# Kernel optimization log

Hardware: AMD Instinct MI355X
Metric: run time of the kernel (lower is better)

Reference implementation:

```python
import jax, jax.numpy as jnp
import numpy as np

D_MODEL = 2048
N_HEADS = 16
D_K = D_MODEL // N_HEADS
MAX_SEQ_LEN = 2048


def _rotary_tables(dim, max_seq_len):
    angular_freq = (1.0 / 10000.0) ** jnp.linspace(0.0, 1.0, dim // 2, dtype=jnp.float32)
    t = jnp.arange(max_seq_len, dtype=jnp.float32)
    theta = jnp.einsum('i,j->ij', t, angular_freq)  # [S, dk/2]
    return jnp.cos(theta), jnp.sin(theta)


def _apply_rotary(x, cos, sin):
    # x: [B, H, S, dk]; cos/sin: [S, dk/2]
    seq_len = x.shape[-2]
    c = cos[:seq_len][None, None]
    s = sin[:seq_len][None, None]
    x1, x2 = jnp.split(x, 2, axis=-1)
    y1 = x1 * c - x2 * s
    y2 = x1 * s + x2 * c
    return jnp.concatenate([y1, y2], axis=-1).astype(x.dtype)


def setup_inputs() -> dict:
    key = jax.random.key(0)
    k_x, k_qkv, k_o = jax.random.split(key, 3)
    B, S = 2, 2048
    x = jax.random.normal(k_x, (B, S, D_MODEL), dtype=jnp.float32)
    scale = 1.0 / np.sqrt(D_MODEL)
    w_qkv = jax.random.normal(k_qkv, (3 * D_MODEL, D_MODEL), dtype=jnp.float32) * scale
    w_o = jax.random.normal(k_o, (D_MODEL, D_MODEL), dtype=jnp.float32) * scale
    return {"x": x, "w_qkv": w_qkv, "w_o": w_o}


def reference(x, w_qkv, w_o):
    B, S, _ = x.shape
    cos, sin = _rotary_tables(D_K, MAX_SEQ_LEN)
    qkv = jnp.einsum('bsd,ed->bse', x, w_qkv)  # [B, S, 3*d_model]
    qkv = qkv.reshape(B, S, 3, N_HEADS, D_K).transpose(2, 0, 3, 1, 4)  # [3,B,H,S,dk]
    Q, K, V = qkv[0], qkv[1], qkv[2]
    Q = _apply_rotary(Q, cos, sin)
    K = _apply_rotary(K, cos, sin)
    scale = 1.0 / np.sqrt(D_K)
    scores = jnp.einsum('bhqd,bhkd->bhqk', Q, K) * scale
    causal = jnp.tril(jnp.ones((S, S), dtype=bool))
    scores = jnp.where(causal[None, None], scores, jnp.finfo(scores.dtype).min)
    attn = jax.nn.softmax(scores, axis=-1)
    out = jnp.einsum('bhqk,bhkd->bhqd', attn, V)  # [B,H,S,dk]
    out = out.transpose(0, 2, 1, 3).reshape(B, S, D_MODEL)
    return jnp.einsum('bsd,ed->bse', out, w_o)
```

## Files before the change

kernel.cpp:

```cpp
#include <hip/hip_runtime.h>
#include <hip/hip_bf16.h>


typedef __bf16 bf16;
typedef __bf16 bf16x4 __attribute__((ext_vector_type(4)));
typedef __bf16 bf16x8 __attribute__((ext_vector_type(8)));
typedef float f32x4 __attribute__((ext_vector_type(4)));
typedef float f32x16 __attribute__((ext_vector_type(16)));
typedef int i32x4 __attribute__((ext_vector_type(4)));

#define DEV __device__ __forceinline__

DEV void gll16(const void* g, void* lds_base_wave_uniform) {
  __builtin_amdgcn_global_load_lds((const __attribute__((address_space(1))) void*)g,
                                   (__attribute__((address_space(3))) void*)lds_base_wave_uniform,
                                   16, 0, 0);
}

DEV f32x4 mfma16(bf16x8 a, bf16x8 b, f32x4 c) {
  return __builtin_amdgcn_mfma_f32_16x16x32_bf16(a, b, c, 0, 0, 0);
}
DEV f32x16 mfma32(bf16x8 a, bf16x8 b, f32x16 c) {
  return __builtin_amdgcn_mfma_f32_32x32x16_bf16(a, b, c, 0, 0, 0);
}

DEV int pack2(float x, float y) {
  union { bf16 h[2]; int i; } u;
  u.h[0] = (bf16)x; u.h[1] = (bf16)y;
  return u.i;
}

__global__ __launch_bounds__(256) void cvt_f32_bf16(const float* __restrict__ in,
                                                    bf16* __restrict__ out, int n) {
  int i = (blockIdx.x * 256 + threadIdx.x) << 3;
  if (i >= n) return;
  float4 a = *(const float4*)(in + i);
  float4 b = *(const float4*)(in + i + 4);
  bf16x8 o;
  o[0] = (bf16)a.x; o[1] = (bf16)a.y; o[2] = (bf16)a.z; o[3] = (bf16)a.w;
  o[4] = (bf16)b.x; o[5] = (bf16)b.y; o[6] = (bf16)b.z; o[7] = (bf16)b.w;
  *(bf16x8*)(out + i) = o;
}

__global__ __launch_bounds__(256) void rope_table(float* __restrict__ ctab,
                                                  float* __restrict__ stab) {
  int id = blockIdx.x * 256 + threadIdx.x;
  int s = id >> 6, j = id & 63;
  float freq = powf(10000.0f, -(float)j / 63.0f);
  float th = (float)s * freq;
  ctab[id] = cosf(th);
  stab[id] = sinf(th);
}

__global__ __launch_bounds__(256) void rope_apply(bf16* __restrict__ Qb, bf16* __restrict__ Kb,
                                                  const float* __restrict__ ctab,
                                                  const float* __restrict__ stab) {
  const float QSCALE = 0.08838834764831845f * 1.4426950408889634f;
  int id = blockIdx.x * 256 + threadIdx.x;
  const int half = 32 * 2048 * 8;
  bf16* P = (id < half) ? Qb : Kb;
  const float scale = (id < half) ? QSCALE : 1.0f;
  int t = (id < half) ? id : id - half;
  const int d0 = (t & 7) << 3;
  const int s = (t >> 3) & 2047;
  const int bh = t >> 14;
  bf16* p = P + (((size_t)bh * 2048 + s) << 7);
  bf16x8 x1 = *(bf16x8*)(p + d0);
  bf16x8 x2 = *(bf16x8*)(p + d0 + 64);
  float4 ca = *(const float4*)(ctab + (s << 6) + d0);
  float4 cb = *(const float4*)(ctab + (s << 6) + d0 + 4);
  float4 sa = *(const float4*)(stab + (s << 6) + d0);
  float4 sb = *(const float4*)(stab + (s << 6) + d0 + 4);
  const float c[8] = {ca.x, ca.y, ca.z, ca.w, cb.x, cb.y, cb.z, cb.w};
  const float sn[8] = {sa.x, sa.y, sa.z, sa.w, sb.x, sb.y, sb.z, sb.w};
  bf16x8 y1, y2;
#pragma unroll
  for (int j = 0; j < 8; ++j) {
    const float a = (float)x1[j], b = (float)x2[j];
    y1[j] = (bf16)((a * c[j] - b * sn[j]) * scale);
    y2[j] = (bf16)((a * sn[j] + b * c[j]) * scale);
  }
  *(bf16x8*)(p + d0) = y1;
  *(bf16x8*)(p + d0 + 64) = y2;
}

__global__ __launch_bounds__(512, 2) void gemm384(const bf16* __restrict__ A,
                                                  const bf16* __restrict__ Bt,
                                                  bf16* __restrict__ q_out,
                                                  bf16* __restrict__ k_out,
                                                  bf16* __restrict__ v_out) {
  constexpr int K = 2048, NKT = 64;
  constexpr int BUFB = 40960;
  __shared__ char lds[3 * BUFB];
  const int id = blockIdx.x;
  const int swz = (id & 7) * 32 + (id >> 3);
  const int bx = swz & 15, by = swz >> 4;
  const int m0 = by << 8;
  const int n0 = bx * 384;
  const int tid = threadIdx.x, w = tid >> 6, l = tid & 63;
  const int wm = w >> 2, wn = w & 3;
  const int lsl = (l & 7) ^ ((l >> 3) & 7);
  const int srow = ((l >> 3) << 1) + (lsl >> 2);
  const int scol = (lsl & 3) << 3;

  auto STAGE = [&](int t, char* base) {
    const int k0 = t << 5;
#pragma unroll
    for (int c = 0; c < 2; ++c) {
      const int row = (c << 7) + (w << 4) + srow;
      gll16(A + (size_t)(m0 + row) * K + k0 + scol, base + (c << 13) + (w << 10));
    }
#pragma unroll
    for (int c = 0; c < 3; ++c) {
      const int row = (c << 7) + (w << 4) + srow;
      gll16(Bt + (size_t)(n0 + row) * K + k0 + scol, base + 16384 + (c << 13) + (w << 10));
    }
  };

  f32x4 acc[8][6] = {};

  STAGE(0, (char*)lds);
  STAGE(1, (char*)lds + BUFB);
  asm volatile("s_waitcnt vmcnt(5)" ::: "memory");
  __builtin_amdgcn_s_barrier();

#pragma unroll 1
  for (int t = 0, bi = 0, bj = 2; t < NKT; ++t) {
    char* rbase = (char*)lds + bi * BUFB;
    bf16x8 bfr[6];
#pragma unroll
    for (int j = 0; j < 6; ++j) {
      const int row = wn * 96 + (j << 4) + (l & 15);
      const int sr = row >> 1;
      bfr[j] = *(const bf16x8*)(rbase + 16384 + sr * 128 +
                                (((((row & 1) << 2) | (l >> 4)) ^ (sr & 7)) << 4));
    }
    bf16x8 af[4];
#pragma unroll
    for (int i = 0; i < 4; ++i) {
      const int row = (wm << 7) + (i << 4) + (l & 15);
      const int sr = row >> 1;
      af[i] = *(const bf16x8*)(rbase + sr * 128 +
                               (((((row & 1) << 2) | (l >> 4)) ^ (sr & 7)) << 4));
    }
    if (t + 2 < NKT) STAGE(t + 2, (char*)lds + bj * BUFB);
    asm volatile("s_waitcnt lgkmcnt(0)" ::: "memory");
    __builtin_amdgcn_sched_barrier(0);
    __builtin_amdgcn_s_setprio(1);
#pragma unroll
    for (int i = 0; i < 4; ++i)
#pragma unroll
      for (int j = 0; j < 6; ++j)
        acc[i][j] = mfma16(af[i], bfr[j], acc[i][j]);
    __builtin_amdgcn_s_setprio(0);
#pragma unroll
    for (int i = 0; i < 4; ++i) {
      const int row = (wm << 7) + 64 + (i << 4) + (l & 15);
      const int sr = row >> 1;
      af[i] = *(const bf16x8*)(rbase + sr * 128 +
                               (((((row & 1) << 2) | (l >> 4)) ^ (sr & 7)) << 4));
    }
    asm volatile("s_waitcnt lgkmcnt(0)" ::: "memory");
    __builtin_amdgcn_sched_barrier(0);
    __builtin_amdgcn_s_setprio(1);
#pragma unroll
    for (int i = 0; i < 4; ++i)
#pragma unroll
      for (int j = 0; j < 6; ++j)
        acc[4 + i][j] = mfma16(af[i], bfr[j], acc[4 + i][j]);
    __builtin_amdgcn_s_setprio(0);
    if (t + 2 < NKT) {
      asm volatile("s_waitcnt vmcnt(5)" ::: "memory");
    } else if (t + 2 == NKT) {
      asm volatile("s_waitcnt vmcnt(0)" ::: "memory");
    }
    __builtin_amdgcn_sched_barrier(0);
    __builtin_amdgcn_s_barrier();
    bi = (bi == 2) ? 0 : bi + 1;
    bj = (bj == 2) ? 0 : bj + 1;
  }

#pragma unroll
  for (int i = 0; i < 8; ++i)
#pragma unroll
    for (int j = 0; j < 6; ++j) {
      const int nl = n0 + wn * 96 + (j << 4) + (l & 15);
      const int which = nl >> 11;
      const int h = (nl >> 7) & 15, d = nl & 127;
      if (which < 2) {
        bf16* dst = which ? k_out : q_out;
#pragma unroll
        for (int r = 0; r < 4; ++r) {
          const int m = m0 + (wm << 7) + (i << 4) + ((l >> 4) << 2) + r;
          const int b_ = m >> 11, s = m & 2047;
          dst[(((size_t)((b_ << 4) | h)) * 2048 + s) * 128 + d] = (bf16)acc[i][j][r];
        }
      } else {
        const int sb = m0 + (wm << 7) + (i << 4) + ((l >> 4) << 2);
        const int b_ = sb >> 11, s = sb & 2047;
        bf16x4 vv;
#pragma unroll
        for (int r = 0; r < 4; ++r) vv[r] = (bf16)acc[i][j][r];
        *(bf16x4*)(v_out + ((size_t)((b_ << 4) | h) << 18) + ((size_t)d << 11) + s) = vv;
      }
    }
}

template <int NTN>
__global__ __launch_bounds__(256, 2) void gemm_o(const bf16* __restrict__ A,
                                                 const bf16* __restrict__ Bt,
                                                 float* __restrict__ f_out) {
  constexpr int K = 2048, NKT = 64;
  constexpr int BUFB = 16384;
  __shared__ char lds[3 * BUFB];
  const int nwg = 32 * NTN;
  const int id = blockIdx.x;
  const int swz = (id & 7) * (nwg >> 3) + (id >> 3);
  const int bx = swz % NTN, by = swz / NTN;
  const int m0 = by << 7, n0 = bx << 7;
  const int tid = threadIdx.x, w = tid >> 6, l = tid & 63;
  const int wm = w >> 1, wn = w & 1;
  const int lsl = (l & 7) ^ ((l >> 3) & 7);
  const int srow = ((l >> 3) << 1) + (lsl >> 2);
  const int scol = (lsl & 3) << 3;

  auto STAGE = [&](int t, char* base) {
    const int k0 = t << 5;
#pragma unroll
    for (int c = 0; c < 2; ++c) {
      const int row = (c << 6) + (w << 4) + srow;
      gll16(A + (size_t)(m0 + row) * K + k0 + scol, base + (c << 12) + (w << 10));
      gll16(Bt + (size_t)(n0 + row) * K + k0 + scol, base + 8192 + (c << 12) + (w << 10));
    }
  };

  f32x4 acc[4][4] = {};

  STAGE(0, (char*)lds);
  STAGE(1, (char*)lds + BUFB);
  asm volatile("s_waitcnt vmcnt(4)" ::: "memory");
  __builtin_amdgcn_s_barrier();

#pragma unroll 1
  for (int t = 0, bi = 0, bj = 2; t < NKT; ++t) {
    char* rbase = (char*)lds + bi * BUFB;
    bf16x8 af[4], bfr[4];
#pragma unroll
    for (int i = 0; i < 4; ++i) {
      const int row = (wm << 6) + (i << 4) + (l & 15);
      const int sr = row >> 1;
      af[i] = *(const bf16x8*)(rbase + sr * 128 +
                               (((((row & 1) << 2) | (l >> 4)) ^ (sr & 7)) << 4));
    }
#pragma unroll
    for (int j = 0; j < 4; ++j) {
      const int row = (wn << 6) + (j << 4) + (l & 15);
      const int sr = row >> 1;
      bfr[j] = *(const bf16x8*)(rbase + 8192 + sr * 128 +
                                (((((row & 1) << 2) | (l >> 4)) ^ (sr & 7)) << 4));
    }
    if (t + 2 < NKT) STAGE(t + 2, (char*)lds + bj * BUFB);
    asm volatile("s_waitcnt lgkmcnt(0)" ::: "memory");
    __builtin_amdgcn_sched_barrier(0);
    __builtin_amdgcn_s_setprio(1);
#pragma unroll
    for (int i = 0; i < 4; ++i)
#pragma unroll
      for (int j = 0; j < 4; ++j)
        acc[i][j] = mfma16(af[i], bfr[j], acc[i][j]);
    __builtin_amdgcn_s_setprio(0);
    if (t + 2 < NKT) {
      asm volatile("s_waitcnt vmcnt(4)" ::: "memory");
    } else if (t + 2 == NKT) {
      asm volatile("s_waitcnt vmcnt(0)" ::: "memory");
    }
    __builtin_amdgcn_sched_barrier(0);
    __builtin_amdgcn_s_barrier();
    bi = (bi == 2) ? 0 : bi + 1;
    bj = (bj == 2) ? 0 : bj + 1;
  }

#pragma unroll
  for (int i = 0; i < 4; ++i)
#pragma unroll
    for (int j = 0; j < 4; ++j)
#pragma unroll
      for (int r = 0; r < 4; ++r) {
        const int m = m0 + (wm << 6) + (i << 4) + ((l >> 4) << 2) + r;
        const int n = n0 + (wn << 6) + (j << 4) + (l & 15);
        f_out[(size_t)m * 2048 + n] = acc[i][j][r];
      }
}

__global__ __launch_bounds__(256, 2) void attn_kernel(const bf16* __restrict__ Qb,
                                                      const bf16* __restrict__ Kb,
                                                      const bf16* __restrict__ Vt,
                                                      bf16* __restrict__ Ao) {
  constexpr int S = 2048;
  __shared__ bf16 Ks[2][64 * 128];
  __shared__ bf16 Vs[2][128 * 64];
  const int idx = blockIdx.x;
  const int bh = idx >> 4;
  int qt = idx & 15;
  if (idx & 256) qt = 15 - qt;
  const int q0 = qt << 7;
  const int tid = threadIdx.x, w = tid >> 6, l = tid & 63;
  const int hi = l >> 5;
  const bf16* Qp = Qb + ((size_t)bh << 18);
  const bf16* Kp = Kb + ((size_t)bh << 18);
  const bf16* Vp = Vt + ((size_t)bh << 18);

  auto STAGE_KV = [&](int kv0, int bufi) {
    char* Kbase = (char*)Ks + (bufi << 14);
    char* Vbase = (char*)Vs + (bufi << 14);
#pragma unroll
    for (int i = 0; i < 4; ++i) {
      const int rk = (w << 4) + (i << 2) + (l >> 4);
      gll16(Kp + ((size_t)(kv0 + rk) << 7) + (((l & 15) ^ (rk & 7)) << 3),
            Kbase + (w << 12) + (i << 10));
      const int rv = (w << 5) + (i << 3) + (l >> 3);
      gll16(Vp + (size_t)rv * S + kv0 + (((l & 7) ^ (rv & 7)) << 3),
            Vbase + (w << 12) + (i << 10));
    }
  };

  bf16x8 qf[8];
#pragma unroll
  for (int kt = 0; kt < 8; ++kt)
    qf[kt] = *(const bf16x8*)(Qp + ((size_t)(q0 + (w << 5) + (l & 31)) << 7) + (kt << 4) + (hi << 3));

  f32x16 o[4] = {};
  float mrun = -3e38f, lrun = 0.f;

  const int qminw = q0 + (w << 5);
  const int qmaxw = qminw + 31;
  const int kv_end = q0 + 128;

  STAGE_KV(0, 0);
  __syncthreads();

  int bufi = 0;
#pragma unroll 1
  for (int kv0 = 0; kv0 < kv_end; kv0 += 64, bufi ^= 1) {
    if (kv0 + 64 < kv_end) STAGE_KV(kv0 + 64, bufi ^ 1);
    if (kv0 <= qmaxw) {
      const char* Kbase = (const char*)Ks + (bufi << 14);
      const char* Vbase = (const char*)Vs + (bufi << 14);
      f32x16 sc0 = {}, sc1 = {};
      __builtin_amdgcn_s_setprio(1);
#pragma unroll
      for (int kt = 0; kt < 8; ++kt) {
        const int rk0 = l & 31;
        const int coff = ((kt << 5) + (hi << 4));
        bf16x8 k0 = *(const bf16x8*)(Kbase + (rk0 << 8) + (coff ^ ((rk0 & 7) << 4)));
        bf16x8 k1 = *(const bf16x8*)(Kbase + ((rk0 + 32) << 8) + (coff ^ ((rk0 & 7) << 4)));
        sc0 = mfma32(k0, qf[kt], sc0);
        sc1 = mfma32(k1, qf[kt], sc1);
      }
      __builtin_amdgcn_s_setprio(0);
      if (kv0 + 63 > qminw) {
        const int qg = qminw + (l & 31);
#pragma unroll
        for (int r = 0; r < 16; ++r) {
          const int kvr = kv0 + (r & 3) + ((r >> 2) << 3) + (hi << 2);
          if (kvr > qg) sc0[r] = -3e38f;
          if (kvr + 32 > qg) sc1[r] = -3e38f;
        }
      }
      float mx = -3e38f;
#pragma unroll
      for (int r = 0; r < 16; ++r) mx = fmaxf(mx, fmaxf(sc0[r], sc1[r]));
      mx = fmaxf(mx, __shfl_xor(mx, 32));
      const float mnew = fmaxf(mrun, mx);
      if (!__all(mx <= mrun)) {
        const float alpha = exp2f(mrun - mnew);
        lrun *= alpha;
#pragma unroll
        for (int dt = 0; dt < 4; ++dt) o[dt] *= alpha;
      }
      mrun = mnew;
      float ps = 0.f;
#pragma unroll
      for (int r = 0; r < 16; ++r) {
        sc0[r] = exp2f(sc0[r] - mnew); ps += sc0[r];
        sc1[r] = exp2f(sc1[r] - mnew); ps += sc1[r];
      }
      ps += __shfl_xor(ps, 32);
      lrun += ps;
#pragma unroll
      for (int ks = 0; ks < 4; ++ks) {
        const f32x16& s = (ks & 2) ? sc1 : sc0;
        const int rb = (ks & 1) << 3;
        int pa_ = pack2(s[rb + 0], s[rb + 1]);
        int pb_ = pack2(s[rb + 2], s[rb + 3]);
        int pc_ = pack2(s[rb + 4], s[rb + 5]);
        int pd_ = pack2(s[rb + 6], s[rb + 7]);
        int sa = __shfl_xor(pa_, 32), sb = __shfl_xor(pb_, 32);
        int sc_ = __shfl_xor(pc_, 32), sd = __shfl_xor(pd_, 32);
        i32x4 pi;
        pi[0] = hi ? sc_ : pa_;
        pi[1] = hi ? sd : pb_;
        pi[2] = hi ? pc_ : sa;
        pi[3] = hi ? pd_ : sb;
        const bf16x8 pf = __builtin_bit_cast(bf16x8, pi);
        __builtin_amdgcn_s_setprio(1);
#pragma unroll
        for (int dt = 0; dt < 4; ++dt) {
          const int rd = (dt << 5) + (l & 31);
          const bf16x8 vf = *(const bf16x8*)(Vbase + (rd << 7) +
                                             (((ks << 5) + (hi << 4)) ^ ((rd & 7) << 4)));
          o[dt] = mfma32(vf, pf, o[dt]);
        }
        __builtin_amdgcn_s_setprio(0);
      }
    }
    __syncthreads();
  }
  const float rinv = 1.0f / lrun;
  const int b = bh >> 4, h = bh & 15;
  const int qg = q0 + (w << 5) + (l & 31);
  bf16* Arow = Ao + (((size_t)(b * S + qg)) << 11) + (h << 7);
#pragma unroll
  for (int dt = 0; dt < 4; ++dt)
#pragma unroll
    for (int g = 0; g < 4; ++g) {
      bf16x4 ov;
#pragma unroll
      for (int r = 0; r < 4; ++r) ov[r] = (bf16)(o[dt][(g << 2) + r] * rinv);
      *(bf16x4*)(Arow + (dt << 5) + (g << 3) + (hi << 2)) = ov;
    }
}

extern "C" void kernel_launch(void* const* d_in, const int* in_sizes, int n_in,
                              void* d_out, int out_size, void* d_ws, size_t ws_size,
                              hipStream_t stream) {
  const float* x = (const float*)d_in[0];
  const float* w_qkv = (const float*)d_in[1];
  const float* w_o = (const float*)d_in[2];
  float* out = (float*)d_out;
  char* ws = (char*)d_ws;

  bf16* xb    = (bf16*)(ws);
  bf16* wqkvb = (bf16*)(ws + (16ull << 20));
  bf16* wob   = (bf16*)(ws + (40ull << 20));
  bf16* Qb    = (bf16*)(ws + (48ull << 20));
  bf16* Kb    = (bf16*)(ws + (64ull << 20));
  bf16* Vt    = (bf16*)(ws + (80ull << 20));
  bf16* Ao    = (bf16*)(ws + (96ull << 20));
  float* ctab = (float*)(ws + (112ull << 20));
  float* stab = (float*)(ws + (113ull << 20));

  cvt_f32_bf16<<<4096, 256, 0, stream>>>(x, xb, 2 * 2048 * 2048);
  cvt_f32_bf16<<<6144, 256, 0, stream>>>(w_qkv, wqkvb, 6144 * 2048);
  cvt_f32_bf16<<<2048, 256, 0, stream>>>(w_o, wob, 2048 * 2048);
  rope_table<<<512, 256, 0, stream>>>(ctab, stab);
  gemm384<<<256, 512, 0, stream>>>(xb, wqkvb, Qb, Kb, Vt);
  rope_apply<<<4096, 256, 0, stream>>>(Qb, Kb, ctab, stab);
  attn_kernel<<<512, 256, 0, stream>>>(Qb, Kb, Vt, Ao);
  gemm_o<16><<<512, 256, 0, stream>>>(Ao, wob, out);
}
```

Baseline: 258.3 us.

## Fuse prep kernels, swizzle attention block order, use packed bf16 convert

Merges the three f32->bf16 conversion launches and the rope table launch into one kernel with block-range dispatch, which removes launch overhead and the gaps between kernels. Remaps attention block indices so that consecutive blocks land on different (bh, qt) pairs, aiming for a better causal load balance across CUs. Replaces the union-based bf16 packing with the v_cvt_pk_bf16_f32 instruction to cut ALU work in the softmax-to-PV path. Rounding behaviour of the inline asm may differ slightly from the scalar casts.

```diff
diff --git a/kernel.cpp b/kernel.cpp
--- a/kernel.cpp
+++ b/kernel.cpp
@@ -24,32 +24,47 @@
   return __builtin_amdgcn_mfma_f32_32x32x16_bf16(a, b, c, 0, 0, 0);
 }
 
-DEV int pack2(float x, float y) {
-  union { bf16 h[2]; int i; } u;
-  u.h[0] = (bf16)x; u.h[1] = (bf16)y;
-  return u.i;
-}
-
-__global__ __launch_bounds__(256) void cvt_f32_bf16(const float* __restrict__ in,
-                                                    bf16* __restrict__ out, int n) {
-  int i = (blockIdx.x * 256 + threadIdx.x) << 3;
-  if (i >= n) return;
-  float4 a = *(const float4*)(in + i);
-  float4 b = *(const float4*)(in + i + 4);
-  bf16x8 o;
-  o[0] = (bf16)a.x; o[1] = (bf16)a.y; o[2] = (bf16)a.z; o[3] = (bf16)a.w;
-  o[4] = (bf16)b.x; o[5] = (bf16)b.y; o[6] = (bf16)b.z; o[7] = (bf16)b.w;
-  *(bf16x8*)(out + i) = o;
-}
-
-__global__ __launch_bounds__(256) void rope_table(float* __restrict__ ctab,
-                                                  float* __restrict__ stab) {
-  int id = blockIdx.x * 256 + threadIdx.x;
-  int s = id >> 6, j = id & 63;
-  float freq = powf(10000.0f, -(float)j / 63.0f);
-  float th = (float)s * freq;
-  ctab[id] = cosf(th);
-  stab[id] = sinf(th);
+DEV int cvtpk(float lo, float hi) {
+  int r;
+  asm("v_cvt_pk_bf16_f32 %0, %1, %2" : "=v"(r) : "v"(lo), "v"(hi));
+  return r;
+}
+
+__global__ __launch_bounds__(256) void prep_all(const float* __restrict__ x,
+                                                const float* __restrict__ wqkv,
+                                                const float* __restrict__ wo,
+                                                bf16* __restrict__ xb,
+                                                bf16* __restrict__ wqkvb,
+                                                bf16* __restrict__ wob,
+                                                float* __restrict__ ctab,
+                                                float* __restrict__ stab) {
+  const int b = blockIdx.x;
+  if (b < 12288) {
+    const float* in;
+    bf16* out;
+    int bb = b;
+    if (b < 4096) {
+      in = x; out = xb;
+    } else if (b < 10240) {
+      in = wqkv; out = wqkvb; bb -= 4096;
+    } else {
+      in = wo; out = wob; bb -= 10240;
+    }
+    const int i = (bb * 256 + threadIdx.x) << 3;
+    float4 a = *(const float4*)(in + i);
+    float4 c = *(const float4*)(in + i + 4);
+    bf16x8 o;
+    o[0] = (bf16)a.x; o[1] = (bf16)a.y; o[2] = (bf16)a.z; o[3] = (bf16)a.w;
+    o[4] = (bf16)c.x; o[5] = (bf16)c.y; o[6] = (bf16)c.z; o[7] = (bf16)c.w;
+    *(bf16x8*)(out + i) = o;
+  } else {
+    const int id = (b - 12288) * 256 + threadIdx.x;
+    const int s = id >> 6, j = id & 63;
+    float freq = powf(10000.0f, -(float)j / 63.0f);
+    float th = (float)s * freq;
+    ctab[id] = cosf(th);
+    stab[id] = sinf(th);
+  }
 }
 
 __global__ __launch_bounds__(256) void rope_apply(bf16* __restrict__ Qb, bf16* __restrict__ Kb,
@@ -299,10 +314,11 @@
   constexpr int S = 2048;
   __shared__ bf16 Ks[2][64 * 128];
   __shared__ bf16 Vs[2][128 * 64];
-  const int idx = blockIdx.x;
-  const int bh = idx >> 4;
-  int qt = idx & 15;
-  if (idx & 256) qt = 15 - qt;
+  const int id = blockIdx.x;
+  const int swz = (id & 7) * 64 + (id >> 3);
+  const int bh = swz >> 4;
+  int qt = swz & 15;
+  if ((swz >> 5) & 1) qt = 15 - qt;
   const int q0 = qt << 7;
   const int tid = threadIdx.x, w = tid >> 6, l = tid & 63;
   const int hi = l >> 5;
@@ -391,10 +407,10 @@
       for (int ks = 0; ks < 4; ++ks) {
         const f32x16& s = (ks & 2) ? sc1 : sc0;
         const int rb = (ks & 1) << 3;
-        int pa_ = pack2(s[rb + 0], s[rb + 1]);
-        int pb_ = pack2(s[rb + 2], s[rb + 3]);
-        int pc_ = pack2(s[rb + 4], s[rb + 5]);
-        int pd_ = pack2(s[rb + 6], s[rb + 7]);
+        int pa_ = cvtpk(s[rb + 0], s[rb + 1]);
+        int pb_ = cvtpk(s[rb + 2], s[rb + 3]);
+        int pc_ = cvtpk(s[rb + 4], s[rb + 5]);
+        int pd_ = cvtpk(s[rb + 6], s[rb + 7]);
         int sa = __shfl_xor(pa_, 32), sb = __shfl_xor(pb_, 32);
         int sc_ = __shfl_xor(pc_, 32), sd = __shfl_xor(pd_, 32);
         i32x4 pi;
@@ -450,10 +466,7 @@
   float* ctab = (float*)(ws + (112ull << 20));
   float* stab = (float*)(ws + (113ull << 20));
 
-  cvt_f32_bf16<<<4096, 256, 0, stream>>>(x, xb, 2 * 2048 * 2048);
-  cvt_f32_bf16<<<6144, 256, 0, stream>>>(w_qkv, wqkvb, 6144 * 2048);
-  cvt_f32_bf16<<<2048, 256, 0, stream>>>(w_o, wob, 2048 * 2048);
-  rope_table<<<512, 256, 0, stream>>>(ctab, stab);
+  prep_all<<<12800, 256, 0, stream>>>(x, w_qkv, w_o, xb, wqkvb, wob, ctab, stab);
   gemm384<<<256, 512, 0, stream>>>(xb, wqkvb, Qb, Kb, Vt);
   rope_apply<<<4096, 256, 0, stream>>>(Qb, Kb, ctab, stab);
   attn_kernel<<<512, 256, 0, stream>>>(Qb, Kb, Vt, Ao);
```

New measurement: 250.0 us. 3.2% less time.
